# Performance work log

Measured on AMD Instinct MI355X. Metric: run time of the kernel, lower is better.

Reference implementation:

```python
import jax, jax.numpy as jnp
import numpy as np

WINDOW_SIZE = 11
CHANNEL = 3
SIGMA = 1.5
C1 = 0.01 ** 2
C2 = 0.03 ** 2


def _gaussian_window():
    # 1D gaussian, normalized, then outer product -> [C,1,K,K] depthwise kernel
    x = np.arange(WINDOW_SIZE, dtype=np.float32)
    g = np.exp(-(x - WINDOW_SIZE // 2) ** 2 / (2.0 * SIGMA ** 2))
    g = g / g.sum()
    w2d = np.outer(g, g).astype(np.float32)  # [K,K]
    w = np.broadcast_to(w2d, (CHANNEL, 1, WINDOW_SIZE, WINDOW_SIZE)).copy()
    return jnp.asarray(w)


def _depthwise_conv(x, w):
    # x: [N,C,H,W], w: [C,1,K,K]; SAME padding (pad = K//2, K odd) matches torch
    pad = WINDOW_SIZE // 2
    return jax.lax.conv_general_dilated(
        x, w,
        window_strides=(1, 1),
        padding=((pad, pad), (pad, pad)),
        dimension_numbers=("NCHW", "OIHW", "NCHW"),
        feature_group_count=CHANNEL,
    )


def setup_inputs() -> dict:
    key = jax.random.key(0)
    kA, kB = jax.random.split(key)
    shape = (16, 3, 512, 512)
    A = jax.random.uniform(kA, shape, dtype=jnp.float32)
    B = jax.random.uniform(kB, shape, dtype=jnp.float32)
    return {"A": A, "B": B}


def reference(A, B):
    w = _gaussian_window()
    mu1 = _depthwise_conv(A, w)
    mu2 = _depthwise_conv(B, w)
    mu1_sq = mu1 * mu1
    mu2_sq = mu2 * mu2
    mu12 = mu1 * mu2
    sigma1_sq = _depthwise_conv(A * A, w) - mu1_sq
    sigma2_sq = _depthwise_conv(B * B, w) - mu2_sq
    sigma12 = _depthwise_conv(A * B, w) - mu12
    num = (2.0 * mu12 + C1) * (2.0 * sigma12 + C2)
    den = (mu1_sq + mu2_sq + C1) * (sigma1_sq + sigma2_sq + C2)
    ssim_map = num / den
    return jnp.nanmean(ssim_map)
```

## Files before the change

kernel.cpp:

```cpp
#include <hip/hip_runtime.h>
#include <math.h>


#define TX 64
#define TY 32
#define SR 42
#define HSTRIDE 65
#define IMG_H 512
#define IMG_W 512
#define C1F 1.0e-4f
#define C2F 9.0e-4f

__global__ void ssim_zero(double* acc) { *acc = 0.0; }

__global__ void ssim_finalize(const double* acc, float* out) {
    *out = (float)(*acc / 12582912.0);
}

__global__ __launch_bounds__(256, 3)
void ssim_main(const float* __restrict__ A, const float* __restrict__ B,
               double* __restrict__ acc)
{
    __shared__ float h[5][SR * HSTRIDE];

    const int t  = threadIdx.x;
    const int x0 = blockIdx.x * TX;
    const int y0 = blockIdx.y * TY;
    const size_t pbase = (size_t)blockIdx.z * (size_t)(IMG_H * IMG_W);
    const float* __restrict__ pa = A + pbase;
    const float* __restrict__ pb = B + pbase;

    float g[11];
    {
        float gs = 0.f;
        #pragma unroll
        for (int i = 0; i < 11; ++i) {
            const float d = (float)(i - 5);
            g[i] = expf(-d * d / 4.5f);
            gs += g[i];
        }
        #pragma unroll
        for (int i = 0; i < 11; ++i) g[i] /= gs;
    }

    if (t < 168) {
        const int r   = t >> 2;
        const int c0  = (t & 3) << 4;
        const int gy  = y0 - 5 + r;
        const int gxb = x0 - 5 + c0;
        const bool rowok = ((unsigned)gy < (unsigned)IMG_H);
        const float* __restrict__ ra = pa + (ptrdiff_t)gy * IMG_W;
        const float* __restrict__ rb = pb + (ptrdiff_t)gy * IMG_W;

        float a[26], b[26];
        if (rowok && gxb >= 0 && gxb + 25 < IMG_W) {
            #pragma unroll
            for (int j = 0; j < 26; ++j) {
                a[j] = ra[gxb + j];
                b[j] = rb[gxb + j];
            }
        } else {
            #pragma unroll
            for (int j = 0; j < 26; ++j) {
                const int gx = gxb + j;
                const bool ok = rowok && ((unsigned)gx < (unsigned)IMG_W);
                a[j] = ok ? ra[gx] : 0.f;
                b[j] = ok ? rb[gx] : 0.f;
            }
        }

        #pragma unroll
        for (int p = 0; p < 16; ++p) {
            float sa = 0.f, sb = 0.f, saa = 0.f, sbb = 0.f, sab = 0.f;
            #pragma unroll
            for (int k = 0; k < 11; ++k) {
                const float w  = g[k];
                const float av = a[p + k];
                const float bv = b[p + k];
                sa  += w * av;
                sb  += w * bv;
                saa += w * (av * av);
                sbb += w * (bv * bv);
                sab += w * (av * bv);
            }
            const int o = r * HSTRIDE + c0 + p;
            h[0][o] = sa;  h[1][o] = sb;
            h[2][o] = saa; h[3][o] = sbb; h[4][o] = sab;
        }
    }
    __syncthreads();

    float lsum = 0.f;
    {
        const int x  = t & 63;
        const int yb = (t >> 6) << 3;
        float m1[8], m2[8], ea[8], eb[8], ec[8];
        #pragma unroll
        for (int j = 0; j < 8; ++j) { m1[j]=0.f; m2[j]=0.f; ea[j]=0.f; eb[j]=0.f; ec[j]=0.f; }

        #pragma unroll
        for (int k = 0; k < 18; ++k) {
            const int o = (yb + k) * HSTRIDE + x;
            const float vA  = h[0][o];
            const float vB  = h[1][o];
            const float vAA = h[2][o];
            const float vBB = h[3][o];
            const float vAB = h[4][o];
            #pragma unroll
            for (int j = 0; j < 8; ++j) {
                const int kk = k - j;
                if (kk >= 0 && kk < 11) {
                    const float w = g[kk];
                    m1[j] += w * vA;  m2[j] += w * vB;
                    ea[j] += w * vAA; eb[j] += w * vBB; ec[j] += w * vAB;
                }
            }
        }

        #pragma unroll
        for (int j = 0; j < 8; ++j) {
            const float mu1 = m1[j], mu2 = m2[j];
            const float mu1s = mu1 * mu1, mu2s = mu2 * mu2, mu12 = mu1 * mu2;
            const float s1  = ea[j] - mu1s;
            const float s2  = eb[j] - mu2s;
            const float s12 = ec[j] - mu12;
            const float num = (2.f * mu12 + C1F) * (2.f * s12 + C2F);
            const float den = (mu1s + mu2s + C1F) * (s1 + s2 + C2F);
            lsum += num / den;
        }
    }

    #pragma unroll
    for (int off = 32; off > 0; off >>= 1)
        lsum += __shfl_down(lsum, off, 64);

    __syncthreads();
    if ((t & 63) == 0) h[0][t >> 6] = lsum;
    __syncthreads();
    if (t == 0) {
        const double bs = (double)h[0][0] + (double)h[0][1]
                        + (double)h[0][2] + (double)h[0][3];
        atomicAdd(acc, bs);
    }
}

extern "C" void kernel_launch(void* const* d_in, const int* in_sizes, int n_in,
                              void* d_out, int out_size, void* d_ws, size_t ws_size,
                              hipStream_t stream) {
    const float* A = (const float*)d_in[0];
    const float* B = (const float*)d_in[1];
    float* out  = (float*)d_out;
    double* acc = (double*)d_ws;

    ssim_zero<<<dim3(1), dim3(1), 0, stream>>>(acc);
    dim3 grid(IMG_W / TX, IMG_H / TY, 48);
    ssim_main<<<grid, dim3(256), 0, stream>>>(A, B, acc);
    ssim_finalize<<<dim3(1), dim3(1), 0, stream>>>(acc, out);
}
```

Before: 186.6 us.

## Spread horizontal pass over more threads, interleave smem layout, shard atomic accumulator

The horizontal blur pass now uses 252 threads, each producing 11 outputs from a 21-wide register window with scatter-style accumulation, instead of 168 threads producing 16 outputs each. The five horizontal planes are interleaved per row with stride 324. The final divide becomes a fast reciprocal with one Newton step, and block sums go to 64 padded atomic slots that a 64-thread finalize kernel reduces. The aim is better thread utilisation in the first phase and less atomic contention, at the cost of more redundant loads from overlapping windows and slightly different rounding.

```diff
diff --git a/kernel.cpp b/kernel.cpp
--- a/kernel.cpp
+++ b/kernel.cpp
@@ -2,90 +2,116 @@
 #include <math.h>
 
 
-#define TX 64
-#define TY 32
-#define SR 42
-#define HSTRIDE 65
-#define IMG_H 512
-#define IMG_W 512
+#define IMG 512
 #define C1F 1.0e-4f
 #define C2F 9.0e-4f
 
-__global__ void ssim_zero(double* acc) { *acc = 0.0; }
+#define SR 42
+#define RS 324
 
-__global__ void ssim_finalize(const double* acc, float* out) {
-    *out = (float)(*acc / 12582912.0);
+__global__ void ssim_zero(double* acc) {
+    if (threadIdx.x < 64) acc[(size_t)threadIdx.x * 8] = 0.0;
+}
+
+__global__ void ssim_finalize(const double* __restrict__ acc, float* __restrict__ out) {
+    double v = acc[(size_t)threadIdx.x * 8];
+    #pragma unroll
+    for (int off = 32; off > 0; off >>= 1)
+        v += __shfl_down(v, off, 64);
+    if (threadIdx.x == 0) *out = (float)(v / 12582912.0);
+}
+
+__device__ __forceinline__ void make_weights(float* g) {
+    float e[6];
+    #pragma unroll
+    for (int k = 0; k < 6; ++k) {
+        const float d = (float)k;
+        e[k] = expf(-d * d / 4.5f);
+    }
+    float gs = e[5];
+    gs += e[4]; gs += e[3]; gs += e[2]; gs += e[1]; gs += e[0];
+    gs += e[1]; gs += e[2]; gs += e[3]; gs += e[4]; gs += e[5];
+    float q[6];
+    #pragma unroll
+    for (int k = 0; k < 6; ++k) q[k] = e[k] / gs;
+    #pragma unroll
+    for (int i = 0; i < 11; ++i) {
+        const int d = (i < 5) ? (5 - i) : (i - 5);
+        g[i] = q[d];
+    }
 }
 
 __global__ __launch_bounds__(256, 3)
 void ssim_main(const float* __restrict__ A, const float* __restrict__ B,
                double* __restrict__ acc)
 {
-    __shared__ float h[5][SR * HSTRIDE];
+    __shared__ float hbuf[SR * RS];
 
     const int t  = threadIdx.x;
-    const int x0 = blockIdx.x * TX;
-    const int y0 = blockIdx.y * TY;
-    const size_t pbase = (size_t)blockIdx.z * (size_t)(IMG_H * IMG_W);
+    const int x0 = blockIdx.x * 64;
+    const int y0 = blockIdx.y * 32;
+    const size_t pbase = (size_t)blockIdx.z * (size_t)(IMG * IMG);
     const float* __restrict__ pa = A + pbase;
     const float* __restrict__ pb = B + pbase;
 
     float g[11];
-    {
-        float gs = 0.f;
-        #pragma unroll
-        for (int i = 0; i < 11; ++i) {
-            const float d = (float)(i - 5);
-            g[i] = expf(-d * d / 4.5f);
-            gs += g[i];
-        }
-        #pragma unroll
-        for (int i = 0; i < 11; ++i) g[i] /= gs;
-    }
+    make_weights(g);
 
-    if (t < 168) {
-        const int r   = t >> 2;
-        const int c0  = (t & 3) << 4;
+    if (t < 252) {
+        const int r = t / 6;
+        const int s = t - 6 * r;
+        const int start = (s == 5) ? 53 : s * 11;
         const int gy  = y0 - 5 + r;
-        const int gxb = x0 - 5 + c0;
-        const bool rowok = ((unsigned)gy < (unsigned)IMG_H);
-        const float* __restrict__ ra = pa + (ptrdiff_t)gy * IMG_W;
-        const float* __restrict__ rb = pb + (ptrdiff_t)gy * IMG_W;
+        const int gx0 = x0 + start - 5;
+        const bool rowok = ((unsigned)gy < (unsigned)IMG);
+        const float* __restrict__ ra = pa + (ptrdiff_t)gy * IMG;
+        const float* __restrict__ rb = pb + (ptrdiff_t)gy * IMG;
 
-        float a[26], b[26];
-        if (rowok && gxb >= 0 && gxb + 25 < IMG_W) {
+        float wa[21], wb[21];
+        if (rowok && gx0 >= 0 && gx0 + 20 < IMG) {
             #pragma unroll
-            for (int j = 0; j < 26; ++j) {
-                a[j] = ra[gxb + j];
-                b[j] = rb[gxb + j];
+            for (int j = 0; j < 21; ++j) {
+                wa[j] = ra[gx0 + j];
+                wb[j] = rb[gx0 + j];
             }
         } else {
             #pragma unroll
-            for (int j = 0; j < 26; ++j) {
-                const int gx = gxb + j;
-                const bool ok = rowok && ((unsigned)gx < (unsigned)IMG_W);
-                a[j] = ok ? ra[gx] : 0.f;
-                b[j] = ok ? rb[gx] : 0.f;
+            for (int j = 0; j < 21; ++j) {
+                const int gx = gx0 + j;
+                const bool ok = rowok && ((unsigned)gx < (unsigned)IMG);
+                wa[j] = ok ? ra[gx] : 0.f;
+                wb[j] = ok ? rb[gx] : 0.f;
             }
         }
 
+        float sa[11], sb[11], saa[11], sbb[11], sab[11];
         #pragma unroll
-        for (int p = 0; p < 16; ++p) {
-            float sa = 0.f, sb = 0.f, saa = 0.f, sbb = 0.f, sab = 0.f;
+        for (int p = 0; p < 11; ++p)
+        { sa[p]=0.f; sb[p]=0.f; saa[p]=0.f; sbb[p]=0.f; sab[p]=0.f; }
+        #pragma unroll
+        for (int m = 0; m < 21; ++m) {
+            const float a = wa[m];
+            const float b = wb[m];
+            const float aa = a * a, bb = b * b, ab = a * b;
             #pragma unroll
-            for (int k = 0; k < 11; ++k) {
-                const float w  = g[k];
-                const float av = a[p + k];
-                const float bv = b[p + k];
-                sa  += w * av;
-                sb  += w * bv;
-                saa += w * (av * av);
-                sbb += w * (bv * bv);
-                sab += w * (av * bv);
+            for (int p = 0; p < 11; ++p) {
+                const int k = m - p;
+                if (k >= 0 && k <= 10) {
+                    const float w = g[k];
+                    sa[p]  += w * a;  sb[p]  += w * b;
+                    saa[p] += w * aa; sbb[p] += w * bb; sab[p] += w * ab;
+                }
             }
-            const int o = r * HSTRIDE + c0 + p;
-            h[0][o] = sa;  h[1][o] = sb;
-            h[2][o] = saa; h[3][o] = sbb; h[4][o] = sab;
+        }
+
+        const int base = r * RS + start;
+        #pragma unroll
+        for (int p = 0; p < 11; ++p) {
+            hbuf[base + p]        = sa[p];
+            hbuf[base + 65 + p]   = sb[p];
+            hbuf[base + 130 + p]  = saa[p];
+            hbuf[base + 195 + p]  = sbb[p];
+            hbuf[base + 260 + p]  = sab[p];
         }
     }
     __syncthreads();
@@ -96,20 +122,21 @@
         const int yb = (t >> 6) << 3;
         float m1[8], m2[8], ea[8], eb[8], ec[8];
         #pragma unroll
-        for (int j = 0; j < 8; ++j) { m1[j]=0.f; m2[j]=0.f; ea[j]=0.f; eb[j]=0.f; ec[j]=0.f; }
+        for (int j = 0; j < 8; ++j)
+        { m1[j]=0.f; m2[j]=0.f; ea[j]=0.f; eb[j]=0.f; ec[j]=0.f; }
 
         #pragma unroll
         for (int k = 0; k < 18; ++k) {
-            const int o = (yb + k) * HSTRIDE + x;
-            const float vA  = h[0][o];
-            const float vB  = h[1][o];
-            const float vAA = h[2][o];
-            const float vBB = h[3][o];
-            const float vAB = h[4][o];
+            const int o = (yb + k) * RS + x;
+            const float vA  = hbuf[o];
+            const float vB  = hbuf[o + 65];
+            const float vAA = hbuf[o + 130];
+            const float vBB = hbuf[o + 195];
+            const float vAB = hbuf[o + 260];
             #pragma unroll
             for (int j = 0; j < 8; ++j) {
                 const int kk = k - j;
-                if (kk >= 0 && kk < 11) {
+                if (kk >= 0 && kk <= 10) {
                     const float w = g[kk];
                     m1[j] += w * vA;  m2[j] += w * vB;
                     ea[j] += w * vAA; eb[j] += w * vBB; ec[j] += w * vAB;
@@ -126,7 +153,9 @@
             const float s12 = ec[j] - mu12;
             const float num = (2.f * mu12 + C1F) * (2.f * s12 + C2F);
             const float den = (mu1s + mu2s + C1F) * (s1 + s2 + C2F);
-            lsum += num / den;
+            float rd = __builtin_amdgcn_rcpf(den);
+            rd = rd * (2.f - den * rd);
+            lsum += num * rd;
         }
     }
 
@@ -135,12 +164,13 @@
         lsum += __shfl_down(lsum, off, 64);
 
     __syncthreads();
-    if ((t & 63) == 0) h[0][t >> 6] = lsum;
+    if ((t & 63) == 0) hbuf[t >> 6] = lsum;
     __syncthreads();
     if (t == 0) {
-        const double bs = (double)h[0][0] + (double)h[0][1]
-                        + (double)h[0][2] + (double)h[0][3];
-        atomicAdd(acc, bs);
+        const double bs = (double)hbuf[0] + (double)hbuf[1]
+                        + (double)hbuf[2] + (double)hbuf[3];
+        const int slot = (blockIdx.x + (blockIdx.y << 3) + (blockIdx.z << 8)) & 63;
+        atomicAdd(&acc[(size_t)slot * 8], bs);
     }
 }
 
@@ -152,8 +182,8 @@
     float* out  = (float*)d_out;
     double* acc = (double*)d_ws;
 
-    ssim_zero<<<dim3(1), dim3(1), 0, stream>>>(acc);
-    dim3 grid(IMG_W / TX, IMG_H / TY, 48);
+    ssim_zero<<<dim3(1), dim3(64), 0, stream>>>(acc);
+    dim3 grid(IMG / 64, IMG / 32, 48);
     ssim_main<<<grid, dim3(256), 0, stream>>>(A, B, acc);
-    ssim_finalize<<<dim3(1), dim3(1), 0, stream>>>(acc, out);
+    ssim_finalize<<<dim3(1), dim3(64), 0, stream>>>(acc, out);
 }
```

Measured after the change: 173.9 us. -6.8%, faster.
